# Performance work log

Hardware: AMD Instinct MI355X
Metric: run time of the kernel (lower is better)

## Reference

```python
import jax, jax.numpy as jnp
import numpy as np
import math

D_MODEL = 1024
N_HEADS = 16
HEAD_DIM = D_MODEL // N_HEADS  # 64
R = HEAD_DIM // 2              # 32
ROPE_BASE = 10000.0
B, T = 4, 2048


def setup_inputs() -> dict:
    key = jax.random.key(0)
    k1, k2, k3, k4, k5 = jax.random.split(key, 5)
    x = jax.random.normal(k1, (B, T, D_MODEL), dtype=jnp.float32)
    Wqkv = jax.random.normal(k2, (3 * D_MODEL, D_MODEL), dtype=jnp.float32) * (1.0 / math.sqrt(D_MODEL))
    Wout = jax.random.normal(k3, (D_MODEL, D_MODEL), dtype=jnp.float32) * (1.0 / math.sqrt(D_MODEL))
    alpha = jax.random.normal(k4, (N_HEADS, R), dtype=jnp.float32) * 0.01
    beta = jax.random.normal(k5, (N_HEADS, R), dtype=jnp.float32) * 0.01
    return {"x": x, "Wqkv": Wqkv, "Wout": Wout, "alpha": alpha, "beta": beta}


def _fourier_bias(alpha, beta, t):
    # omega[r] = base^{-2r/head_dim}, same geometric spacing as RoPE
    omega = ROPE_BASE ** (-2.0 * jnp.arange(R, dtype=jnp.float32) / HEAD_DIM)
    # bias depends only on displacement i-j in [-(t-1), t-1]: compute once per
    # displacement, then gather into the (t, t) matrix (same math as full T x T).
    disp = jnp.arange(-(t - 1), t, dtype=jnp.float32)            # (2t-1,)
    angles = omega[:, None] * disp[None, :]                       # (R, 2t-1)
    vec = jnp.einsum('hr,rk->hk', alpha, jnp.cos(angles)) \
        + jnp.einsum('hr,rk->hk', beta, jnp.sin(angles))          # (H, 2t-1)
    i = jnp.arange(t)
    idx = i[:, None] - i[None, :] + (t - 1)                       # (t, t), delta[i,j]=i-j
    return vec[:, idx]                                            # (H, t, t)


def reference(x, Wqkv, Wout, alpha, beta):
    b, t, d = x.shape
    qkv = x @ Wqkv.T                                              # (B, T, 3D)
    q, k, v = jnp.split(qkv, 3, axis=-1)
    def heads(a):
        return a.reshape(b, t, N_HEADS, HEAD_DIM).transpose(0, 2, 1, 3)  # (B,H,T,dh)
    q, k, v = heads(q), heads(k), heads(v)
    scale = 1.0 / math.sqrt(HEAD_DIM)
    logits = jnp.einsum('bhqd,bhkd->bhqk', q, k) * scale          # (B,H,T,T)
    logits = logits + _fourier_bias(alpha, beta, t)[None]
    causal = jnp.tril(jnp.ones((t, t), dtype=bool))
    logits = jnp.where(causal[None, None], logits, -jnp.inf)
    attn = jax.nn.softmax(logits, axis=-1)
    out = jnp.einsum('bhqk,bhkd->bhqd', attn, v)                  # (B,H,T,dh)
    out = out.transpose(0, 2, 1, 3).reshape(b, t, d)
    return out @ Wout.T
```

## Files before the change

### kernel.cpp

```cpp
#include <hip/hip_runtime.h>
#include <cstdint>
#include <cstddef>

typedef _Float16 f16;
typedef f16 f16x8 __attribute__((ext_vector_type(8)));
typedef __fp16 fp16x2 __attribute__((ext_vector_type(2)));
typedef float f32x4 __attribute__((ext_vector_type(4)));
typedef float f32x16 __attribute__((ext_vector_type(16)));
typedef uint32_t u32;


__device__ __forceinline__ void gload16(const void* g, void* l) {
  __builtin_amdgcn_global_load_lds((const __attribute__((address_space(1))) void*)g,
                                   (__attribute__((address_space(3))) void*)l,
                                   16u, 0, 0u);
}

__device__ __forceinline__ u32 pkrtz(float a, float b) {
  union { fp16x2 v; u32 u; } t;
  t.v = __builtin_amdgcn_cvt_pkrtz(a, b);
  return t.u;
}

__device__ __forceinline__ u32 packh2(float a, float b) { return pkrtz(a, b); }

__device__ __forceinline__ float max3f(float a, float b, float c) {
  return fmaxf(fmaxf(a, b), c);
}

__device__ __forceinline__ void pl32swap(u32& a, u32& b) {
  asm volatile("v_permlane32_swap_b32 %0, %1" : "+v"(a), "+v"(b));
}


__global__ __launch_bounds__(256) void cvt_f32_f16(const float* __restrict__ in,
                                                   f16* __restrict__ out, int n) {
  int i = (blockIdx.x * 256 + threadIdx.x) * 8;
  if (i >= n) return;
  float4 a = *(const float4*)(in + i);
  float4 b = *(const float4*)(in + i + 4);
  f16x8 o;
  o[0] = (f16)a.x; o[1] = (f16)a.y; o[2] = (f16)a.z; o[3] = (f16)a.w;
  o[4] = (f16)b.x; o[5] = (f16)b.y; o[6] = (f16)b.z; o[7] = (f16)b.w;
  *(f16x8*)(out + i) = o;
}


__global__ __launch_bounds__(256) void build_tables(const float* __restrict__ alpha,
                                                    const float* __restrict__ beta,
                                                    f16* __restrict__ U,
                                                    f16* __restrict__ Wt) {
  int idx = blockIdx.x * 256 + threadIdx.x;
  int t = idx >> 5, r = idx & 31;
  float w = powf(10000.0f, -(float)r / 32.0f);
  float ang = w * (float)t;
  float c = cosf(ang), s = sinf(ang);
  const float L2E = 1.44269504089f;
  U[t * 64 + 2 * r]     = (f16)(c * L2E);
  U[t * 64 + 2 * r + 1] = (f16)(s * L2E);
  #pragma unroll
  for (int h = 0; h < 16; ++h) {
    float al = alpha[h * 32 + r], be = beta[h * 32 + r];
    Wt[(size_t)(h * 2048 + t) * 64 + 2 * r]     = (f16)(al * c - be * s);
    Wt[(size_t)(h * 2048 + t) * 64 + 2 * r + 1] = (f16)(al * s + be * c);
  }
}


__global__ __launch_bounds__(256) void gemm_qkv(const f16* __restrict__ A,
                                                const f16* __restrict__ B,
                                                f16* __restrict__ Q,
                                                f16* __restrict__ Kh,
                                                f16* __restrict__ Vt) {
  __shared__ __align__(16) char sm[32768];
  char* As = sm;
  char* Bs = sm + 16384;
  const int K = 1024;
  int tid = threadIdx.x;
  int lane = tid & 63, wid = tid >> 6;
  int bid = blockIdx.x;
  int id = (bid & 7) * 192 + (bid >> 3);
  int m0 = (id / 24) * 128, n0 = (id % 24) * 128;
  int wm = wid >> 1, wn = wid & 1;
  int c = lane & 15, g = lane >> 4, l7 = lane & 7;

  f32x4 acc[4][4] = {};

  for (int kt = 0; kt < K / 64; ++kt) {
    #pragma unroll
    for (int i = 0; i < 4; ++i) {
      int p = i * 4096 + tid * 16;
      int q = p ^ (((p >> 7) & 7) << 4);
      int row = q >> 7, ce = (q & 127) >> 1;
      gload16(A + (size_t)(m0 + row) * K + kt * 64 + ce, As + i * 4096 + wid * 1024);
      gload16(B + (size_t)(n0 + row) * K + kt * 64 + ce, Bs + i * 4096 + wid * 1024);
    }
    __syncthreads();
    #pragma unroll
    for (int kk = 0; kk < 2; ++kk) {
      int co = (kk * 64 + g * 16) ^ (l7 << 4);
      f16x8 af[4], bf[4];
      #pragma unroll
      for (int fr = 0; fr < 4; ++fr)
        af[fr] = *(const f16x8*)(As + (wm * 64 + fr * 16 + c) * 128 + co);
      #pragma unroll
      for (int fn = 0; fn < 4; ++fn)
        bf[fn] = *(const f16x8*)(Bs + (wn * 64 + fn * 16 + c) * 128 + co);
      #pragma unroll
      for (int fr = 0; fr < 4; ++fr)
        #pragma unroll
        for (int fn = 0; fn < 4; ++fn)
          acc[fr][fn] = __builtin_amdgcn_mfma_f32_16x16x32_f16(af[fr], bf[fn], acc[fr][fn], 0, 0, 0);
    }
    __syncthreads();
  }

  int which = n0 >> 10;
  #pragma unroll
  for (int fr = 0; fr < 4; ++fr) {
    int m = m0 + wm * 64 + fr * 16 + g * 4;
    int b = m >> 11, t = m & 2047;
    #pragma unroll
    for (int fn = 0; fn < 4; ++fn) {
      int n = n0 + wn * 64 + fn * 16 + c;
      int nf = n & 1023, hh = nf >> 6, d = nf & 63;
      if (which == 0) {
        #pragma unroll
        for (int r = 0; r < 4; ++r)
          Q[(size_t)((b * 16 + hh) * 2048 + (t + r)) * 64 + d] = (f16)(acc[fr][fn][r] * 0.180336880111f);
      } else if (which == 1) {
        #pragma unroll
        for (int r = 0; r < 4; ++r)
          Kh[(size_t)((b * 16 + hh) * 2048 + (t + r)) * 64 + d] = (f16)acc[fr][fn][r];
      } else {
        uint2 pk;
        pk.x = packh2(acc[fr][fn][0], acc[fr][fn][1]);
        pk.y = packh2(acc[fr][fn][2], acc[fr][fn][3]);
        *(uint2*)(Vt + (size_t)((b * 16 + hh) * 64 + d) * 2048 + t) = pk;
      }
    }
  }
}


__global__ __launch_bounds__(256) void gemm_out(const f16* __restrict__ A,
                                                const f16* __restrict__ B,
                                                float* __restrict__ Cout) {
  __shared__ __align__(16) char sm[32768];
  char* As = sm;
  char* Bs = sm + 16384;
  const int K = 1024;
  int tid = threadIdx.x;
  int lane = tid & 63, wid = tid >> 6;
  int bid = blockIdx.x;
  int id = (bid & 7) * 64 + (bid >> 3);
  int m0 = (id >> 3) * 128, n0 = (id & 7) * 128;
  int wm = wid >> 1, wn = wid & 1;
  int c = lane & 15, g = lane >> 4, l7 = lane & 7;

  f32x4 acc[4][4] = {};

  for (int kt = 0; kt < K / 64; ++kt) {
    #pragma unroll
    for (int i = 0; i < 4; ++i) {
      int p = i * 4096 + tid * 16;
      int q = p ^ (((p >> 7) & 7) << 4);
      int row = q >> 7, ce = (q & 127) >> 1;
      gload16(A + (size_t)(m0 + row) * K + kt * 64 + ce, As + i * 4096 + wid * 1024);
      gload16(B + (size_t)(n0 + row) * K + kt * 64 + ce, Bs + i * 4096 + wid * 1024);
    }
    __syncthreads();
    #pragma unroll
    for (int kk = 0; kk < 2; ++kk) {
      int co = (kk * 64 + g * 16) ^ (l7 << 4);
      f16x8 af[4], bf[4];
      #pragma unroll
      for (int fr = 0; fr < 4; ++fr)
        af[fr] = *(const f16x8*)(As + (wm * 64 + fr * 16 + c) * 128 + co);
      #pragma unroll
      for (int fn = 0; fn < 4; ++fn)
        bf[fn] = *(const f16x8*)(Bs + (wn * 64 + fn * 16 + c) * 128 + co);
      #pragma unroll
      for (int fr = 0; fr < 4; ++fr)
        #pragma unroll
        for (int fn = 0; fn < 4; ++fn)
          acc[fr][fn] = __builtin_amdgcn_mfma_f32_16x16x32_f16(af[fr], bf[fn], acc[fr][fn], 0, 0, 0);
    }
    __syncthreads();
  }

  #pragma unroll
  for (int fr = 0; fr < 4; ++fr) {
    int m = m0 + wm * 64 + fr * 16 + g * 4;
    #pragma unroll
    for (int fn = 0; fn < 4; ++fn) {
      int n = n0 + wn * 64 + fn * 16 + c;
      #pragma unroll
      for (int r = 0; r < 4; ++r)
        Cout[(size_t)(m + r) * 1024 + n] = acc[fr][fn][r];
    }
  }
}


__global__ __launch_bounds__(512, 2) void attn(const f16* __restrict__ Q,
                                               const f16* __restrict__ Kh,
                                               const f16* __restrict__ Vt,
                                               const f16* __restrict__ U,
                                               const f16* __restrict__ Wt,
                                               f16* __restrict__ AO) {
  __shared__ __align__(16) char sm[49152];
  int tid = threadIdx.x, lane = tid & 63, wid = tid >> 6;
  int l31 = lane & 31, hi = lane >> 5;
  int o = blockIdx.x;
  int pr = o >> 6;
  int bh = o & 63;
  int h = bh & 15, b = bh >> 4;
  int swzK = (lane & 15) << 4;
  int swzV = (lane & 7) << 4;

  const f16* ksrc[2]; int kdst[2];
  #pragma unroll
  for (int i = 0; i < 2; ++i) {
    int p = i * 8192 + tid * 16;
    int row = p >> 8;
    int col = (p & 255) ^ ((row & 15) << 4);
    int ce = col >> 1;
    ksrc[i] = (ce < 64) ? (Kh + (size_t)(bh * 2048 + row) * 64 + ce)
                        : (Wt + (size_t)(h * 2048 + row) * 64 + (ce - 64));
    kdst[i] = i * 8192 + (tid >> 6) * 1024;
  }
  const f16* vsrc; int vdst;
  {
    int p = tid * 16;
    int row = p >> 7;
    int col = (p & 127) ^ ((row & 7) << 4);
    int ce = col >> 1;
    vsrc = Vt + (size_t)(bh * 64 + row) * 2048 + ce;
    vdst = (tid >> 6) * 1024;
  }

  #pragma unroll 1
  for (int pass = 0; pass < 2; ++pass) {
    int qt = pass ? pr : 7 - pr;
    int qrow = qt * 256 + wid * 32 + l31;
    int ktmax = 4 * qt + 3;

    f16x8 qf[8];
    {
      const f16* qp = Q + (size_t)(bh * 2048 + qrow) * 64 + hi * 8;
      const f16* up = U + (size_t)qrow * 64 + hi * 8;
      #pragma unroll
      for (int ks = 0; ks < 4; ++ks) {
        qf[ks]     = *(const f16x8*)(qp + ks * 16);
        qf[4 + ks] = *(const f16x8*)(up + ks * 16);
      }
    }

    float m_i = -1e30f, l_i = 0.0f;
    f32x16 accA = {}, accB = {};

    #pragma unroll
    for (int i = 0; i < 2; ++i) gload16(ksrc[i], sm + kdst[i]);
    gload16(vsrc, sm + 32768 + vdst);
    __syncthreads();

    for (int kt = 0; kt <= ktmax; ++kt) {
      int cur = kt & 1;
      char* Ks = sm + cur * 16384;
      char* Vs = sm + 32768 + cur * 8192;

      if (kt < ktmax) {
        char* kb = sm + (cur ^ 1) * 16384;
        char* vb = sm + 32768 + (cur ^ 1) * 8192;
        #pragma unroll
        for (int i = 0; i < 2; ++i) gload16(ksrc[i] + (size_t)(kt + 1) * 4096, kb + kdst[i]);
        gload16(vsrc + (size_t)(kt + 1) * 64, vb + vdst);
      }

      f32x16 st0 = {}, st1 = {};
      __builtin_amdgcn_s_setprio(1);
      #pragma unroll
      for (int ks = 0; ks < 8; ++ks) {
        int co = (ks * 32 + hi * 16) ^ swzK;
        f16x8 k0 = *(const f16x8*)(Ks + l31 * 256 + co);
        f16x8 k1 = *(const f16x8*)(Ks + (32 + l31) * 256 + co);
        st0 = __builtin_amdgcn_mfma_f32_32x32x16_f16(k0, qf[ks], st0, 0, 0, 0);
        st1 = __builtin_amdgcn_mfma_f32_32x32x16_f16(k1, qf[ks], st1, 0, 0, 0);
      }
      __builtin_amdgcn_s_setprio(0);

      int kv0 = kt * 64;
      if (kv0 + 63 > qt * 256 + wid * 32) {
        #pragma unroll
        for (int r = 0; r < 16; ++r) {
          int kvl = kv0 + (r & 3) + 8 * (r >> 2) + 4 * hi;
          if (kvl > qrow) st0[r] = -1e30f;
          if (kvl + 32 > qrow) st1[r] = -1e30f;
        }
      }

      float pm = fmaxf(st0[0], st1[0]);
      #pragma unroll
      for (int r = 1; r < 16; ++r) pm = max3f(pm, st0[r], st1[r]);
      pm = fmaxf(pm, __shfl_xor(pm, 32, 64));
      if (!__all(pm <= m_i + 8.0f)) {
        float mnew = fmaxf(m_i, pm);
        float sc = __builtin_amdgcn_exp2f(m_i - mnew);
        l_i *= sc;
        accA *= sc;
        accB *= sc;
        m_i = mnew;
      }

      float ps = 0.0f;
      u32 pk0[8], pk1[8];
      #pragma unroll
      for (int j = 0; j < 8; ++j) {
        float a0 = __builtin_amdgcn_exp2f(st0[2 * j] - m_i);
        float a1 = __builtin_amdgcn_exp2f(st0[2 * j + 1] - m_i);
        float b0 = __builtin_amdgcn_exp2f(st1[2 * j] - m_i);
        float b1 = __builtin_amdgcn_exp2f(st1[2 * j + 1] - m_i);
        ps += (a0 + a1) + (b0 + b1);
        pk0[j] = pkrtz(a0, a1);
        pk1[j] = pkrtz(b0, b1);
      }
      ps += __shfl_xor(ps, 32, 64);
      l_i += ps;

      pl32swap(pk0[0], pk0[2]); pl32swap(pk0[1], pk0[3]);
      pl32swap(pk0[4], pk0[6]); pl32swap(pk0[5], pk0[7]);
      pl32swap(pk1[0], pk1[2]); pl32swap(pk1[1], pk1[3]);
      pl32swap(pk1[4], pk1[6]); pl32swap(pk1[5], pk1[7]);

      __builtin_amdgcn_s_setprio(1);
      #pragma unroll
      for (int kb = 0; kb < 4; ++kb) {
        union { u32 w[4]; f16x8 v; } bf;
        if (kb == 0)      { bf.w[0] = pk0[0]; bf.w[1] = pk0[1]; bf.w[2] = pk0[2]; bf.w[3] = pk0[3]; }
        else if (kb == 1) { bf.w[0] = pk0[4]; bf.w[1] = pk0[5]; bf.w[2] = pk0[6]; bf.w[3] = pk0[7]; }
        else if (kb == 2) { bf.w[0] = pk1[0]; bf.w[1] = pk1[1]; bf.w[2] = pk1[2]; bf.w[3] = pk1[3]; }
        else              { bf.w[0] = pk1[4]; bf.w[1] = pk1[5]; bf.w[2] = pk1[6]; bf.w[3] = pk1[7]; }
        int co = (kb * 32 + hi * 16) ^ swzV;
        f16x8 v0 = *(const f16x8*)(Vs + l31 * 128 + co);
        f16x8 v1 = *(const f16x8*)(Vs + (32 + l31) * 128 + co);
        accA = __builtin_amdgcn_mfma_f32_32x32x16_f16(v0, bf.v, accA, 0, 0, 0);
        accB = __builtin_amdgcn_mfma_f32_32x32x16_f16(v1, bf.v, accB, 0, 0, 0);
      }
      __builtin_amdgcn_s_setprio(0);
      __syncthreads();
    }

    float inv = __builtin_amdgcn_rcpf(l_i);
    f16* aop = AO + (size_t)(b * 2048 + qrow) * 1024 + h * 64;
    #pragma unroll
    for (int u = 0; u < 4; ++u) {
      uint2 ov;
      ov.x = pkrtz(accA[4 * u] * inv, accA[4 * u + 1] * inv);
      ov.y = pkrtz(accA[4 * u + 2] * inv, accA[4 * u + 3] * inv);
      *(uint2*)(aop + 8 * u + 4 * hi) = ov;
      ov.x = pkrtz(accB[4 * u] * inv, accB[4 * u + 1] * inv);
      ov.y = pkrtz(accB[4 * u + 2] * inv, accB[4 * u + 3] * inv);
      *(uint2*)(aop + 32 + 8 * u + 4 * hi) = ov;
    }
  }
}


extern "C" void kernel_launch(void* const* d_in, const int* in_sizes, int n_in,
                              void* d_out, int out_size, void* d_ws, size_t ws_size,
                              hipStream_t stream) {
  const float* x     = (const float*)d_in[0];
  const float* Wqkv  = (const float*)d_in[1];
  const float* Wout  = (const float*)d_in[2];
  const float* alpha = (const float*)d_in[3];
  const float* beta  = (const float*)d_in[4];

  char* ws = (char*)d_ws;
  f16* Xh    = (f16*)(ws);
  f16* Wqkvh = (f16*)(ws + 16777216);
  f16* Wouth = (f16*)(ws + 23068672);
  f16* Qh    = (f16*)(ws + 25165824);
  f16* Kh    = (f16*)(ws + 41943040);
  f16* Vt    = (f16*)(ws + 58720256);
  f16* U     = (f16*)(ws + 75497472);
  f16* Wt    = (f16*)(ws + 75759616);
  f16* AO    = Xh;

  cvt_f32_f16<<<4096, 256, 0, stream>>>(x, Xh, 8388608);
  cvt_f32_f16<<<1536, 256, 0, stream>>>(Wqkv, Wqkvh, 3145728);
  cvt_f32_f16<<<512, 256, 0, stream>>>(Wout, Wouth, 1048576);
  build_tables<<<256, 256, 0, stream>>>(alpha, beta, U, Wt);
  gemm_qkv<<<1536, 256, 0, stream>>>(Xh, Wqkvh, Qh, Kh, Vt);
  attn<<<256, 512, 0, stream>>>(Qh, Kh, Vt, U, Wt, AO);
  gemm_out<<<512, 256, 0, stream>>>(AO, Wouth, (float*)d_out);
}
```

Before: 184.4 us.

## Double-buffer LDS in QKV and output GEMMs with XCD-aware tile mapping

Both projection GEMMs now use two LDS stages, prefetching the next K-tile with global_load_lds while MFMAs run on the current one, and raise wave priority during the MFMA section. The block-to-tile mapping is changed so each XCD owns a fixed set of N columns, which should improve L2 reuse of the weight tiles. The cost is doubled LDS per block (64KB), which may reduce occupancy. The loop also drops the barrier between the loads and the MFMAs, relying on the trailing barrier of the previous iteration; this is correct only if global_load_lds data is visible to the wave by the time that barrier passes.

```diff
diff --git a/kernel.cpp b/kernel.cpp
--- a/kernel.cpp
+++ b/kernel.cpp
@@ -72,30 +72,53 @@
                                                 f16* __restrict__ Q,
                                                 f16* __restrict__ Kh,
                                                 f16* __restrict__ Vt) {
-  __shared__ __align__(16) char sm[32768];
-  char* As = sm;
-  char* Bs = sm + 16384;
+  __shared__ __align__(16) char sm[65536];
   const int K = 1024;
   int tid = threadIdx.x;
   int lane = tid & 63, wid = tid >> 6;
   int bid = blockIdx.x;
-  int id = (bid & 7) * 192 + (bid >> 3);
-  int m0 = (id / 24) * 128, n0 = (id % 24) * 128;
+  int xcd = bid & 7;
+  int id = bid >> 3;
+  int nl = id / 64;
+  int m0 = (id & 63) * 128;
+  int n0 = (xcd * 3 + nl) * 128;
   int wm = wid >> 1, wn = wid & 1;
   int c = lane & 15, g = lane >> 4, l7 = lane & 7;
 
+  int srow[4], sce[4], sdst[4];
+  #pragma unroll
+  for (int i = 0; i < 4; ++i) {
+    int p = i * 4096 + tid * 16;
+    int q = p ^ (((p >> 7) & 7) << 4);
+    srow[i] = q >> 7; sce[i] = (q & 127) >> 1;
+    sdst[i] = i * 4096 + wid * 1024;
+  }
+
   f32x4 acc[4][4] = {};
 
-  for (int kt = 0; kt < K / 64; ++kt) {
-    #pragma unroll
-    for (int i = 0; i < 4; ++i) {
-      int p = i * 4096 + tid * 16;
-      int q = p ^ (((p >> 7) & 7) << 4);
-      int row = q >> 7, ce = (q & 127) >> 1;
-      gload16(A + (size_t)(m0 + row) * K + kt * 64 + ce, As + i * 4096 + wid * 1024);
-      gload16(B + (size_t)(n0 + row) * K + kt * 64 + ce, Bs + i * 4096 + wid * 1024);
-    }
-    __syncthreads();
+  #pragma unroll
+  for (int i = 0; i < 4; ++i) {
+    gload16(A + (size_t)(m0 + srow[i]) * K + sce[i], sm + sdst[i]);
+    gload16(B + (size_t)(n0 + srow[i]) * K + sce[i], sm + 32768 + sdst[i]);
+  }
+  __syncthreads();
+
+  for (int kt = 0; kt < 16; ++kt) {
+    int cur = kt & 1;
+    char* As = sm + cur * 16384;
+    char* Bs = sm + 32768 + cur * 16384;
+
+    if (kt < 15) {
+      char* Ad = sm + (cur ^ 1) * 16384;
+      char* Bd = sm + 32768 + (cur ^ 1) * 16384;
+      #pragma unroll
+      for (int i = 0; i < 4; ++i) {
+        gload16(A + (size_t)(m0 + srow[i]) * K + (kt + 1) * 64 + sce[i], Ad + sdst[i]);
+        gload16(B + (size_t)(n0 + srow[i]) * K + (kt + 1) * 64 + sce[i], Bd + sdst[i]);
+      }
+    }
+
+    __builtin_amdgcn_s_setprio(1);
     #pragma unroll
     for (int kk = 0; kk < 2; ++kk) {
       int co = (kk * 64 + g * 16) ^ (l7 << 4);
@@ -112,6 +135,7 @@
         for (int fn = 0; fn < 4; ++fn)
           acc[fr][fn] = __builtin_amdgcn_mfma_f32_16x16x32_f16(af[fr], bf[fn], acc[fr][fn], 0, 0, 0);
     }
+    __builtin_amdgcn_s_setprio(0);
     __syncthreads();
   }
 
@@ -146,30 +170,52 @@
 __global__ __launch_bounds__(256) void gemm_out(const f16* __restrict__ A,
                                                 const f16* __restrict__ B,
                                                 float* __restrict__ Cout) {
-  __shared__ __align__(16) char sm[32768];
-  char* As = sm;
-  char* Bs = sm + 16384;
+  __shared__ __align__(16) char sm[65536];
   const int K = 1024;
   int tid = threadIdx.x;
   int lane = tid & 63, wid = tid >> 6;
   int bid = blockIdx.x;
-  int id = (bid & 7) * 64 + (bid >> 3);
-  int m0 = (id >> 3) * 128, n0 = (id & 7) * 128;
+  int xcd = bid & 7;
+  int id = bid >> 3;
+  int m0 = id * 128;
+  int n0 = xcd * 128;
   int wm = wid >> 1, wn = wid & 1;
   int c = lane & 15, g = lane >> 4, l7 = lane & 7;
 
+  int srow[4], sce[4], sdst[4];
+  #pragma unroll
+  for (int i = 0; i < 4; ++i) {
+    int p = i * 4096 + tid * 16;
+    int q = p ^ (((p >> 7) & 7) << 4);
+    srow[i] = q >> 7; sce[i] = (q & 127) >> 1;
+    sdst[i] = i * 4096 + wid * 1024;
+  }
+
   f32x4 acc[4][4] = {};
 
-  for (int kt = 0; kt < K / 64; ++kt) {
-    #pragma unroll
-    for (int i = 0; i < 4; ++i) {
-      int p = i * 4096 + tid * 16;
-      int q = p ^ (((p >> 7) & 7) << 4);
-      int row = q >> 7, ce = (q & 127) >> 1;
-      gload16(A + (size_t)(m0 + row) * K + kt * 64 + ce, As + i * 4096 + wid * 1024);
-      gload16(B + (size_t)(n0 + row) * K + kt * 64 + ce, Bs + i * 4096 + wid * 1024);
-    }
-    __syncthreads();
+  #pragma unroll
+  for (int i = 0; i < 4; ++i) {
+    gload16(A + (size_t)(m0 + srow[i]) * K + sce[i], sm + sdst[i]);
+    gload16(B + (size_t)(n0 + srow[i]) * K + sce[i], sm + 32768 + sdst[i]);
+  }
+  __syncthreads();
+
+  for (int kt = 0; kt < 16; ++kt) {
+    int cur = kt & 1;
+    char* As = sm + cur * 16384;
+    char* Bs = sm + 32768 + cur * 16384;
+
+    if (kt < 15) {
+      char* Ad = sm + (cur ^ 1) * 16384;
+      char* Bd = sm + 32768 + (cur ^ 1) * 16384;
+      #pragma unroll
+      for (int i = 0; i < 4; ++i) {
+        gload16(A + (size_t)(m0 + srow[i]) * K + (kt + 1) * 64 + sce[i], Ad + sdst[i]);
+        gload16(B + (size_t)(n0 + srow[i]) * K + (kt + 1) * 64 + sce[i], Bd + sdst[i]);
+      }
+    }
+
+    __builtin_amdgcn_s_setprio(1);
     #pragma unroll
     for (int kk = 0; kk < 2; ++kk) {
       int co = (kk * 64 + g * 16) ^ (l7 << 4);
@@ -186,6 +232,7 @@
         for (int fn = 0; fn < 4; ++fn)
           acc[fr][fn] = __builtin_amdgcn_mfma_f32_16x16x32_f16(af[fr], bf[fn], acc[fr][fn], 0, 0, 0);
     }
+    __builtin_amdgcn_s_setprio(0);
     __syncthreads();
   }
 
```

Result: no change. 188.0 us (+2.0%).
